# Performance work log

Hardware: AMD Instinct MI355X
Metric: run time of the kernel (lower is better)

## Reference

```python
import jax, jax.numpy as jnp
import numpy as np

SCALES = [1.0, 0.9, 0.8, 0.7, 0.6]  # [1 - i/10 for i in range(level=5)]
RES_SCALE = 1.0


def conv2d(x, w, b, pad):
    # NCHW conv, OIHW weights, stride 1, symmetric padding
    y = jax.lax.conv_general_dilated(
        x, w, window_strides=(1, 1), padding=[(pad, pad), (pad, pad)],
        dimension_numbers=("NCHW", "OIHW", "NCHW"))
    return y + b[None, :, None, None]


def _cubic_kernel(d, a=-0.75):
    # torch-style bicubic kernel (a = -0.75)
    d = jnp.abs(d)
    w1 = ((a + 2.0) * d - (a + 3.0)) * d * d + 1.0          # |d| <= 1
    w2 = (((a * d) - 5.0 * a) * d + 8.0 * a) * d - 4.0 * a  # 1 < |d| < 2
    return jnp.where(d <= 1.0, w1, jnp.where(d < 2.0, w2, 0.0))


def _resize_axis(x, out_size, axis):
    in_size = x.shape[axis]
    scale = in_size / out_size
    src = (jnp.arange(out_size, dtype=jnp.float32) + 0.5) * scale - 0.5  # align_corners=False
    x0 = jnp.floor(src)
    t = src - x0
    x0 = x0.astype(jnp.int32)
    out = 0.0
    bshape = [1] * x.ndim
    bshape[axis] = out_size
    for off in range(-1, 3):
        idx = jnp.clip(x0 + off, 0, in_size - 1)  # border replicate
        wgt = _cubic_kernel(t - off).reshape(bshape)
        out = out + jnp.take(x, idx, axis=axis) * wgt
    return out


def bicubic(x, oh, ow):
    return _resize_axis(_resize_axis(x, oh, 2), ow, 3)


def setup_inputs() -> dict:
    key = jax.random.key(0)
    ks = jax.random.split(key, 7)
    C, Cr = 64, 32  # channel=64, reduction=2
    x = jax.random.normal(ks[0], (4, C, 48, 48), dtype=jnp.float32)
    wb = jax.random.normal(ks[1], (Cr, C, 3, 3), dtype=jnp.float32) * 0.05  # conv_match_L_base
    bb = jax.random.normal(ks[2], (Cr,), dtype=jnp.float32) * 0.05
    wm = jax.random.normal(ks[3], (Cr, C, 3, 3), dtype=jnp.float32) * 0.05  # conv_match
    bm = jax.random.normal(ks[4], (Cr,), dtype=jnp.float32) * 0.05
    wa = jax.random.normal(ks[5], (C, C, 1, 1), dtype=jnp.float32) * 0.05   # conv_assembly
    ba = jax.random.normal(ks[6], (C,), dtype=jnp.float32) * 0.05
    return {"x": x, "wb": wb, "bb": bb, "wm": wm, "bm": bm, "wa": wa, "ba": ba}


def reference(x, wb, bb, wm, bm, wa, ba):
    N, C, H, W = x.shape
    mb = conv2d(x, wb, bb, 1)                           # [N,Cr,H,W]
    Cr = mb.shape[1]
    mb = mb.reshape(N, Cr, H * W).transpose(0, 2, 1)    # [N,HW,Cr]  (queries)
    raws, keys = [], []
    for s in SCALES:
        ref = x if s == 1.0 else bicubic(x, int(H * s), int(W * s))
        raws.append(conv2d(ref, wa, ba, 0).reshape(N, C, -1))   # values [N,C,HiWi]
        keys.append(conv2d(ref, wm, bm, 1).reshape(N, Cr, -1))  # keys   [N,Cr,HiWi]
    pyr = jnp.concatenate(keys, axis=-1)                        # [N,Cr,L]
    raw = jnp.concatenate(raws, axis=-1).transpose(0, 2, 1)     # [N,L,C]
    score = jax.nn.softmax(jnp.einsum("nqc,ncl->nql", mb, pyr), axis=-1)  # [N,HW,L]
    y = jnp.einsum("nql,nlc->nqc", score, raw)                  # [N,HW,C]
    y = y.transpose(0, 2, 1).reshape(N, C, H, W)
    return y * RES_SCALE + x
```

## Files before the change

kernel.cpp:

```cpp
#include <hip/hip_runtime.h>
#include <math.h>

typedef unsigned short ushort_t;
typedef __attribute__((ext_vector_type(8))) short short8;
typedef __attribute__((ext_vector_type(4))) float float4v;

#define NB 4
#define C 64
#define CR 32
#define HW 2304
#define LTOT 7470
#define LPAD 7472
#define NSEG 15
#define SEG 512
#define LOG2E 1.44269504088896f

#define YP_F 0
#define LP_F 8847360
#define MBBF_F   8985600
#define KEYBF_F  9133056
#define RAWTBF_F 9611136
#define WPK_F    10567552
#define WPQ_F    10576768
#define WPV_F    10585984

static __device__ __forceinline__ ushort_t f2bf(float f) {
  union { float f; unsigned u; } v; v.f = f;
  unsigned r = v.u + 0x7FFF + ((v.u >> 16) & 1);
  return (ushort_t)(r >> 16);
}

__device__ __forceinline__ float cubicw(float d) {
  float ad = fabsf(d);
  float w1 = (1.25f * ad - 2.25f) * ad * ad + 1.0f;
  float w2 = ((-0.75f * ad + 3.75f) * ad - 6.0f) * ad + 3.0f;
  return ad <= 1.0f ? w1 : (ad < 2.0f ? w2 : 0.0f);
}

__global__ __launch_bounds__(256) void k_prep(const float* __restrict__ x,
    const float* __restrict__ wm, const float* __restrict__ wb,
    const float* __restrict__ wa, ushort_t* __restrict__ xt,
    ushort_t* __restrict__ wpk, ushort_t* __restrict__ wpq,
    ushort_t* __restrict__ wpv) {
  __shared__ float tile[64][49];
  int bx = blockIdx.x, t = threadIdx.x;

  if (bx < 98) {
    int item = bx * 256 + t;
    if (item < 24960) {
      int pxslot = item >> 3, c8 = item & 7;
      int n = pxslot / 780, rr = pxslot % 780;
      int Dp, PDD, pixb, r;
      if (rr < 196)      { Dp = 50; PDD = 2500; pixb = 0;     r = rr; }
      else if (rr < 372) { Dp = 45; PDD = 2025; pixb = 10000; r = rr - 196; }
      else if (rr < 528) { Dp = 40; PDD = 1600; pixb = 18100; r = rr - 372; }
      else if (rr < 664) { Dp = 35; PDD = 1225; pixb = 24500; r = rr - 528; }
      else               { Dp = 30; PDD = 900;  pixb = 29400; r = rr - 664; }
      int py, px;
      if (r < Dp)            { py = 0; px = r; }
      else if (r < 2 * Dp)   { py = Dp - 1; px = r - Dp; }
      else { int s = r - 2 * Dp; py = 1 + (s >> 1); px = (s & 1) ? Dp - 1 : 0; }
      uint4 z = {0u, 0u, 0u, 0u};
      *(uint4*)(xt + ((size_t)(pixb + n * PDD + py * Dp + px)) * 64 + c8 * 8) = z;
    }
  } else if (bx < 290) {
    int pb = bx - 98;
    int py = pb % 48, n = pb / 48;
#pragma unroll
    for (int i = 0; i < 12; i++) {
      int idx = i * 256 + t;
      int c = idx / 48, px = idx % 48;
      tile[c][px] = x[(size_t)(n * 64 + c) * HW + py * 48 + px];
    }
    __syncthreads();
#pragma unroll
    for (int i = 0; i < 12; i++) {
      int idx = i * 256 + t;
      int c = idx & 63, px = idx >> 6;
      xt[(size_t)(n * 2500 + (py + 1) * 50 + px + 1) * 64 + c] = f2bf(tile[c][px]);
    }
  } else if (bx < 5456) {
    int tid = (bx - 290) * 256 + t;
    if (tid >= 1322496) return;
    int D, Dp, PDD, rem, pixb;
    if (tid < 473344)       { D = 43; Dp = 45; PDD = 2025; rem = tid;           pixb = 10000; }
    else if (tid < 843008)  { D = 38; Dp = 40; PDD = 1600; rem = tid - 473344;  pixb = 18100; }
    else if (tid < 1121792) { D = 33; Dp = 35; PDD = 1225; rem = tid - 843008;  pixb = 24500; }
    else                    { D = 28; Dp = 30; PDD = 900;  rem = tid - 1121792; pixb = 29400; }
    int DD = D * D;
    int pix = rem % DD, nc = rem / DD;
    int py = pix / D, px = pix % D;
    float scale = 48.0f / (float)D;
    float sy = ((float)py + 0.5f) * scale - 0.5f;
    float sx = ((float)px + 0.5f) * scale - 0.5f;
    float y0f = floorf(sy), x0f = floorf(sx);
    int y0 = (int)y0f, x0 = (int)x0f;
    float ty = sy - y0f, tx = sx - x0f;
    float wy[4], wxv[4];
#pragma unroll
    for (int k = 0; k < 4; k++) {
      wy[k]  = cubicw(ty - (float)(k - 1));
      wxv[k] = cubicw(tx - (float)(k - 1));
    }
    const float* src = x + (size_t)nc * HW;
    float acc = 0.f;
#pragma unroll
    for (int dy = 0; dy < 4; ++dy) {
      int iy = min(max(y0 - 1 + dy, 0), 47);
      const float* row = src + iy * 48;
      float a = 0.f;
#pragma unroll
      for (int dx = 0; dx < 4; ++dx) {
        int ix = min(max(x0 - 1 + dx, 0), 47);
        a = fmaf(wxv[dx], row[ix], a);
      }
      acc = fmaf(wy[dy], a, acc);
    }
    int n = nc >> 6, c = nc & 63;
    xt[(size_t)(pixb + n * PDD + (py + 1) * Dp + (px + 1)) * 64 + c] = f2bf(acc);
  } else {
    int tid = (bx - 5456) * 256 + t;
    if (tid >= 5120) return;
    int lane = tid & 63, col = lane & 15, kg = lane >> 4;
    if (tid < 4608) {
      int f = (tid >> 6) % 36;
      bool isq = tid >= 2304;
      int tap = f >> 2, half = (f >> 1) & 1, crt = f & 1;
      int cr = crt * 16 + col;
      int ic0 = half * 32 + kg * 8;
      const float* w = isq ? wb : wm;
      short8 v;
#pragma unroll
      for (int j = 0; j < 8; j++) v[j] = (short)f2bf(w[cr * 576 + (ic0 + j) * 9 + tap]);
      *(short8*)((isq ? wpq : wpk) + (size_t)f * 512 + lane * 8) = v;
    } else {
      int id = tid - 4608;
      int f = id >> 6;
      int half = f >> 2, vt = f & 3;
      int c = vt * 16 + col, ic0 = half * 32 + kg * 8;
      short8 v;
#pragma unroll
      for (int j = 0; j < 8; j++) v[j] = (short)f2bf(wa[c * 64 + ic0 + j]);
      *(short8*)(wpv + (size_t)f * 512 + lane * 8) = v;
    }
  }
}

__global__ __launch_bounds__(256) void k_conv(const ushort_t* __restrict__ xt,
    const ushort_t* __restrict__ wpk, const ushort_t* __restrict__ wpq,
    const ushort_t* __restrict__ wpv, const float* __restrict__ bm,
    const float* __restrict__ bb, const float* __restrict__ ba,
    ushort_t* __restrict__ keybf, ushort_t* __restrict__ mbbf,
    ushort_t* __restrict__ rawtbf) {
  int t = threadIdx.x;
  int unit = blockIdx.x * 4 + (t >> 6);
  if (unit >= 938) return;
  int lane = t & 63, col = lane & 15, quad = lane >> 4;
  int n = blockIdx.y;
  int tile = unit >> 1, crt = unit & 1;
  int D, Dp, PDD, DD, pixb, lb, tloc;
  if (tile < 144)      { D = 48; Dp = 50; PDD = 2500; DD = 2304; pixb = 0;     lb = 0;    tloc = tile; }
  else if (tile < 260) { D = 43; Dp = 45; PDD = 2025; DD = 1849; pixb = 10000; lb = 2304; tloc = tile - 144; }
  else if (tile < 351) { D = 38; Dp = 40; PDD = 1600; DD = 1444; pixb = 18100; lb = 4153; tloc = tile - 260; }
  else if (tile < 420) { D = 33; Dp = 35; PDD = 1225; DD = 1089; pixb = 24500; lb = 5597; tloc = tile - 351; }
  else                 { D = 28; Dp = 30; PDD = 900;  DD = 784;  pixb = 29400; lb = 6686; tloc = tile - 420; }
  bool lvl0 = (tile < 144);

  int p = tloc * 16 + col;
  int pv = min(p, DD - 1);
  int py = pv / D, px = pv - py * D;
  const ushort_t* xb = xt + ((size_t)(pixb + n * PDD + (py + 1) * Dp + (px + 1))) * 64 + quad * 8;

  float4v Dk = {0.f, 0.f, 0.f, 0.f};
  float4v Dq = {0.f, 0.f, 0.f, 0.f};
  float4v Dv0 = {0.f, 0.f, 0.f, 0.f};
  float4v Dv1 = {0.f, 0.f, 0.f, 0.f};

#pragma unroll
  for (int dy = -1; dy <= 1; dy++) {
#pragma unroll
    for (int dx = -1; dx <= 1; dx++) {
      int tap = (dy + 1) * 3 + (dx + 1);
      const ushort_t* ab = xb + (dy * Dp + dx) * 64;
#pragma unroll
      for (int half = 0; half < 2; half++) {
        short8 A = *(const short8*)(ab + half * 32);
        int f = (tap * 2 + half) * 2 + crt;
        short8 Bk = *(const short8*)(wpk + (size_t)f * 512 + lane * 8);
        Dk = __builtin_amdgcn_mfma_f32_16x16x32_bf16(A, Bk, Dk, 0, 0, 0);
        if (lvl0) {
          short8 Bq = *(const short8*)(wpq + (size_t)f * 512 + lane * 8);
          Dq = __builtin_amdgcn_mfma_f32_16x16x32_bf16(A, Bq, Dq, 0, 0, 0);
        }
        if (tap == 4) {
          short8 Bv0 = *(const short8*)(wpv + (size_t)(half * 4 + crt * 2) * 512 + lane * 8);
          short8 Bv1 = *(const short8*)(wpv + (size_t)(half * 4 + crt * 2 + 1) * 512 + lane * 8);
          Dv0 = __builtin_amdgcn_mfma_f32_16x16x32_bf16(A, Bv0, Dv0, 0, 0, 0);
          Dv1 = __builtin_amdgcn_mfma_f32_16x16x32_bf16(A, Bv1, Dv1, 0, 0, 0);
        }
      }
    }
  }

  float biask = bm[crt * 16 + col];
  float biasq = bb[crt * 16 + col];
  float biasv0 = ba[crt * 32 + col];
  float biasv1 = ba[crt * 32 + 16 + col];
  int prow = tloc * 16 + quad * 4;
#pragma unroll
  for (int r = 0; r < 4; r++) {
    if (prow + r < DD) {
      int l = lb + prow + r;
      keybf[(size_t)(n * LTOT + l) * 32 + crt * 16 + col] = f2bf(Dk[r] + biask);
      if (lvl0) mbbf[(size_t)(n * HW + l) * 32 + crt * 16 + col] = f2bf((Dq[r] + biasq) * LOG2E);
      rawtbf[(size_t)(n * 64 + crt * 32 + col) * LPAD + l] = f2bf(Dv0[r] + biasv0);
      rawtbf[(size_t)(n * 64 + crt * 32 + 16 + col) * LPAD + l] = f2bf(Dv1[r] + biasv1);
    }
  }
}

__global__ __launch_bounds__(256, 4) void k_attn(const ushort_t* __restrict__ mb,
    const ushort_t* __restrict__ keyb, const ushort_t* __restrict__ rawt,
    float* __restrict__ Yp, float* __restrict__ lp) {
  __shared__ __align__(16) ushort_t VsF[2][4096];
  __shared__ __align__(16) ushort_t Pq[4][32 * 72];

  int t = threadIdx.x;
  int n = blockIdx.y, seg = blockIdx.z;
  int lane = t & 63, wv = t >> 6;
  int col = lane & 15, quad = lane >> 4;
  int qb = blockIdx.x * 128 + wv * 32;
  int l_begin = seg * SEG;
  int l_end = min(l_begin + SEG, LTOT);
  int nfull = (l_end - l_begin) >> 6;
  int rem = (l_end - l_begin) & 63;
  int nch = nfull + (rem ? 1 : 0);

  const ushort_t* keyn = keyb + (size_t)n * LTOT * CR;
  const ushort_t* rawn = rawt + (size_t)n * C * LPAD;

  short8 qA0 = *(const short8*)(mb + ((size_t)(n * HW + qb + col)) * CR + quad * 8);
  short8 qA1 = *(const short8*)(mb + ((size_t)(n * HW + qb + 16 + col)) * CR + quad * 8);

  int ct0 = (t >> 6) & 3, g0 = (t >> 4) & 3, cc0 = t & 15;
  size_t so0 = (size_t)(ct0 * 16 + cc0) * LPAD + g0 * 8;

  float4v Y0[4], Y1[4];
#pragma unroll
  for (int ct = 0; ct < 4; ct++)
#pragma unroll
    for (int r = 0; r < 4; r++) { Y0[ct][r] = 0.f; Y1[ct][r] = 0.f; }
  float ls0 = 0.f, ls1 = 0.f;
  const float4v zero4 = {0.f, 0.f, 0.f, 0.f};
  ushort_t* Pw = Pq[wv];

  uint4 va = *(const uint4*)(rawn + so0 + l_begin);
  uint4 vb = *(const uint4*)(rawn + so0 + 32 + l_begin);
  int buf = 0;

  for (int ch = 0; ch < nch; ++ch) {
    int l0 = l_begin + ch * 64;
    *(uint4*)&VsF[buf][t * 8] = va;
    *(uint4*)&VsF[buf][(t + 256) * 8] = vb;
    if (ch + 1 < nch) {
      int ln = l0 + 64;
      va = *(const uint4*)(rawn + so0 + ln);
      vb = *(const uint4*)(rawn + so0 + 32 + ln);
    }
    __syncthreads();

    bool tail = (rem != 0) && (ch == nfull);
#pragma unroll
    for (int tt = 0; tt < 4; tt++) {
      short8 kf = *(const short8*)(keyn + (size_t)(l0 + tt * 16 + col) * CR + quad * 8);
      float4v S0 = __builtin_amdgcn_mfma_f32_16x16x32_bf16(kf, qA0, zero4, 0, 0, 0);
      float4v S1 = __builtin_amdgcn_mfma_f32_16x16x32_bf16(kf, qA1, zero4, 0, 0, 0);
      int lbase = tt * 16 + quad * 4;
      float p0[4], p1[4];
#pragma unroll
      for (int r = 0; r < 4; r++) {
        bool ok = !tail || (lbase + r < rem);
        float a = __builtin_amdgcn_exp2f(S0[r]);
        float b = __builtin_amdgcn_exp2f(S1[r]);
        p0[r] = ok ? a : 0.f;
        p1[r] = ok ? b : 0.f;
        ls0 += p0[r];
        ls1 += p1[r];
      }
      union { float f; unsigned u; } c0, c1;
      uint2 w;
      c0.f = p0[0]; c1.f = p0[1];
      w.x = ((c0.u + 0x8000u) >> 16) | ((c1.u + 0x8000u) & 0xFFFF0000u);
      c0.f = p0[2]; c1.f = p0[3];
      w.y = ((c0.u + 0x8000u) >> 16) | ((c1.u + 0x8000u) & 0xFFFF0000u);
      *(uint2*)&Pw[col * 72 + lbase] = w;
      c0.f = p1[0]; c1.f = p1[1];
      w.x = ((c0.u + 0x8000u) >> 16) | ((c1.u + 0x8000u) & 0xFFFF0000u);
      c0.f = p1[2]; c1.f = p1[3];
      w.y = ((c0.u + 0x8000u) >> 16) | ((c1.u + 0x8000u) & 0xFFFF0000u);
      *(uint2*)&Pw[(16 + col) * 72 + lbase] = w;
    }

#pragma unroll
    for (int kt = 0; kt < 2; kt++) {
      short8 a0 = *(const short8*)&Pw[col * 72 + kt * 32 + quad * 8];
      short8 a1 = *(const short8*)&Pw[(16 + col) * 72 + kt * 32 + quad * 8];
#pragma unroll
      for (int ct = 0; ct < 4; ct++) {
        short8 bV = *(const short8*)&VsF[buf][(((kt << 2) | ct) * 64 + lane) * 8];
        Y0[ct] = __builtin_amdgcn_mfma_f32_16x16x32_bf16(a0, bV, Y0[ct], 0, 0, 0);
        Y1[ct] = __builtin_amdgcn_mfma_f32_16x16x32_bf16(a1, bV, Y1[ct], 0, 0, 0);
      }
    }
    buf ^= 1;
  }

  ls0 += __shfl_xor(ls0, 16); ls0 += __shfl_xor(ls0, 32);
  ls1 += __shfl_xor(ls1, 16); ls1 += __shfl_xor(ls1, 32);

  float* yo = Yp + ((size_t)(seg * NB + n) * HW + qb) * C;
#pragma unroll
  for (int ct = 0; ct < 4; ct++)
#pragma unroll
    for (int r = 0; r < 4; r++) {
      yo[(quad * 4 + r) * C + ct * 16 + col] = Y0[ct][r];
      yo[(16 + quad * 4 + r) * C + ct * 16 + col] = Y1[ct][r];
    }
  if (quad == 0) {
    int base = (seg * NB + n) * HW + qb;
    lp[base + col] = ls0;
    lp[base + 16 + col] = ls1;
  }
}

__global__ void k_combine(const float* __restrict__ x, const float* __restrict__ ws,
                          float* __restrict__ out) {
  int tid = blockIdx.x * 256 + threadIdx.x;
  int c = tid & 63;
  int t2 = tid >> 6;
  int q = t2 % HW;
  int n = t2 / HW;
  const float* Yv = ws + YP_F;
  const float* lpv = ws + LP_F;
  int i0 = n * HW + q;
  float den = 0.f, num = 0.f;
#pragma unroll
  for (int s = 0; s < NSEG; s++) {
    int idx = s * NB * HW + i0;
    den += lpv[idx];
    num += Yv[(size_t)idx * C + c];
  }
  int oi = (n * C + c) * HW + q;
  out[oi] = num / den + x[oi];
}

extern "C" void kernel_launch(void* const* d_in, const int* in_sizes, int n_in,
                              void* d_out, int out_size, void* d_ws, size_t ws_size,
                              hipStream_t stream) {
  const float* x  = (const float*)d_in[0];
  const float* wb = (const float*)d_in[1];
  const float* bb = (const float*)d_in[2];
  const float* wm = (const float*)d_in[3];
  const float* bm = (const float*)d_in[4];
  const float* wa = (const float*)d_in[5];
  const float* ba = (const float*)d_in[6];
  float* out = (float*)d_out;
  float* ws = (float*)d_ws;
  ushort_t* xt     = (ushort_t*)ws;
  ushort_t* mbbf   = (ushort_t*)(ws + MBBF_F);
  ushort_t* keybf  = (ushort_t*)(ws + KEYBF_F);
  ushort_t* rawtbf = (ushort_t*)(ws + RAWTBF_F);
  ushort_t* wpk    = (ushort_t*)(ws + WPK_F);
  ushort_t* wpq    = (ushort_t*)(ws + WPQ_F);
  ushort_t* wpv    = (ushort_t*)(ws + WPV_F);

  k_prep<<<5476, 256, 0, stream>>>(x, wm, wb, wa, xt, wpk, wpq, wpv);
  k_conv<<<dim3(235, 4), 256, 0, stream>>>(xt, wpk, wpq, wpv, bm, bb, ba,
                                           keybf, mbbf, rawtbf);
  k_attn<<<dim3(18, 4, NSEG), 256, 0, stream>>>(mbbf, keybf, rawtbf,
      ws + YP_F, ws + LP_F);
  k_combine<<<2304, 256, 0, stream>>>(x, ws, out);
}
```

Baseline: 147.6 us.

## Load V directly into registers in attention, fewer segments, vectorized combine

```diff
diff --git a/kernel.cpp b/kernel.cpp
--- a/kernel.cpp
+++ b/kernel.cpp
@@ -11,12 +11,12 @@
 #define HW 2304
 #define LTOT 7470
 #define LPAD 7472
-#define NSEG 15
-#define SEG 512
+#define NSEG 10
+#define SEG 768
 #define LOG2E 1.44269504088896f
 
 #define YP_F 0
-#define LP_F 8847360
+#define LP_F 5898240
 #define MBBF_F   8985600
 #define KEYBF_F  9133056
 #define RAWTBF_F 9611136
@@ -219,10 +219,9 @@
   }
 }
 
-__global__ __launch_bounds__(256, 4) void k_attn(const ushort_t* __restrict__ mb,
+__global__ __launch_bounds__(256) void k_attn(const ushort_t* __restrict__ mb,
     const ushort_t* __restrict__ keyb, const ushort_t* __restrict__ rawt,
     float* __restrict__ Yp, float* __restrict__ lp) {
-  __shared__ __align__(16) ushort_t VsF[2][4096];
   __shared__ __align__(16) ushort_t Pq[4][32 * 72];
 
   int t = threadIdx.x;
@@ -242,9 +241,6 @@
   short8 qA0 = *(const short8*)(mb + ((size_t)(n * HW + qb + col)) * CR + quad * 8);
   short8 qA1 = *(const short8*)(mb + ((size_t)(n * HW + qb + 16 + col)) * CR + quad * 8);
 
-  int ct0 = (t >> 6) & 3, g0 = (t >> 4) & 3, cc0 = t & 15;
-  size_t so0 = (size_t)(ct0 * 16 + cc0) * LPAD + g0 * 8;
-
   float4v Y0[4], Y1[4];
 #pragma unroll
   for (int ct = 0; ct < 4; ct++)
@@ -254,27 +250,28 @@
   const float4v zero4 = {0.f, 0.f, 0.f, 0.f};
   ushort_t* Pw = Pq[wv];
 
-  uint4 va = *(const uint4*)(rawn + so0 + l_begin);
-  uint4 vb = *(const uint4*)(rawn + so0 + 32 + l_begin);
-  int buf = 0;
+  const ushort_t* kbase = keyn + (size_t)(l_begin + col) * CR + quad * 8;
+  size_t vrow = (size_t)col * LPAD + quad * 8;
 
   for (int ch = 0; ch < nch; ++ch) {
     int l0 = l_begin + ch * 64;
-    *(uint4*)&VsF[buf][t * 8] = va;
-    *(uint4*)&VsF[buf][(t + 256) * 8] = vb;
-    if (ch + 1 < nch) {
-      int ln = l0 + 64;
-      va = *(const uint4*)(rawn + so0 + ln);
-      vb = *(const uint4*)(rawn + so0 + 32 + ln);
-    }
-    __syncthreads();
-
     bool tail = (rem != 0) && (ch == nfull);
+
+    short8 kf[4];
+#pragma unroll
+    for (int tt = 0; tt < 4; tt++)
+      kf[tt] = *(const short8*)(kbase + (size_t)(ch * 64 + tt * 16) * CR);
+    short8 bv[8];
+#pragma unroll
+    for (int kt = 0; kt < 2; kt++)
+#pragma unroll
+      for (int ct = 0; ct < 4; ct++)
+        bv[(kt << 2) | ct] = *(const short8*)(rawn + vrow + (size_t)ct * 16 * LPAD + l0 + kt * 32);
+
 #pragma unroll
     for (int tt = 0; tt < 4; tt++) {
-      short8 kf = *(const short8*)(keyn + (size_t)(l0 + tt * 16 + col) * CR + quad * 8);
-      float4v S0 = __builtin_amdgcn_mfma_f32_16x16x32_bf16(kf, qA0, zero4, 0, 0, 0);
-      float4v S1 = __builtin_amdgcn_mfma_f32_16x16x32_bf16(kf, qA1, zero4, 0, 0, 0);
+      float4v S0 = __builtin_amdgcn_mfma_f32_16x16x32_bf16(kf[tt], qA0, zero4, 0, 0, 0);
+      float4v S1 = __builtin_amdgcn_mfma_f32_16x16x32_bf16(kf[tt], qA1, zero4, 0, 0, 0);
       int lbase = tt * 16 + quad * 4;
       float p0[4], p1[4];
 #pragma unroll
@@ -307,12 +304,11 @@
       short8 a1 = *(const short8*)&Pw[(16 + col) * 72 + kt * 32 + quad * 8];
 #pragma unroll
       for (int ct = 0; ct < 4; ct++) {
-        short8 bV = *(const short8*)&VsF[buf][(((kt << 2) | ct) * 64 + lane) * 8];
+        short8 bV = bv[(kt << 2) | ct];
         Y0[ct] = __builtin_amdgcn_mfma_f32_16x16x32_bf16(a0, bV, Y0[ct], 0, 0, 0);
         Y1[ct] = __builtin_amdgcn_mfma_f32_16x16x32_bf16(a1, bV, Y1[ct], 0, 0, 0);
       }
     }
-    buf ^= 1;
   }
 
   ls0 += __shfl_xor(ls0, 16); ls0 += __shfl_xor(ls0, 32);
@@ -335,23 +331,29 @@
 
 __global__ void k_combine(const float* __restrict__ x, const float* __restrict__ ws,
                           float* __restrict__ out) {
-  int tid = blockIdx.x * 256 + threadIdx.x;
-  int c = tid & 63;
-  int t2 = tid >> 6;
-  int q = t2 % HW;
-  int n = t2 / HW;
+  int idx = blockIdx.x * 256 + threadIdx.x;
+  int n = idx / 36864;
+  int rm = idx - n * 36864;
+  int c4 = rm / HW;
+  int q = rm - c4 * HW;
   const float* Yv = ws + YP_F;
   const float* lpv = ws + LP_F;
   int i0 = n * HW + q;
-  float den = 0.f, num = 0.f;
+  float den = 0.f;
+  float4v num = {0.f, 0.f, 0.f, 0.f};
 #pragma unroll
   for (int s = 0; s < NSEG; s++) {
-    int idx = s * NB * HW + i0;
-    den += lpv[idx];
-    num += Yv[(size_t)idx * C + c];
-  }
-  int oi = (n * C + c) * HW + q;
-  out[oi] = num / den + x[oi];
+    int base = s * NB * HW + i0;
+    float4v yv = *(const float4v*)(Yv + (size_t)base * C + c4 * 4);
+    num += yv;
+    den += lpv[base];
+  }
+  float inv = 1.0f / den;
+  int ob = (n * C + c4 * 4) * HW + q;
+  out[ob]          = num[0] * inv + x[ob];
+  out[ob + HW]     = num[1] * inv + x[ob + HW];
+  out[ob + 2 * HW] = num[2] * inv + x[ob + 2 * HW];
+  out[ob + 3 * HW] = num[3] * inv + x[ob + 3 * HW];
 }
 
 extern "C" void kernel_launch(void* const* d_in, const int* in_sizes, int n_in,
@@ -379,5 +381,5 @@
                                            keybf, mbbf, rawtbf);
   k_attn<<<dim3(18, 4, NSEG), 256, 0, stream>>>(mbbf, keybf, rawtbf,
       ws + YP_F, ws + LP_F);
-  k_combine<<<2304, 256, 0, stream>>>(x, ws, out);
-}
+  k_combine<<<576, 256, 0, stream>>>(x, ws, out);
+}
```

Result: slower. 170.2 us (+15.3%).
